# Kernel tuning notes

Measured on AMD Instinct MI355X. Metric: run time of the kernel, lower is better.

Reference implementation:

```python
import jax, jax.numpy as jnp
import numpy as np

ORDINAL = 2.0
EPS_INNER = 1e-32 * float(1.0 / ORDINAL < 1.0)  # added to inv_covar**2 (active: 0.5 < 1)
EPS_OUTER = 1e-32 * float(ORDINAL < 1.0)        # inactive for ordinal=2

def setup_inputs() -> dict:
    key = jax.random.key(0)
    k1, k2, k3, k4, k5 = jax.random.split(key, 5)
    B, I, O = 1024, 512, 512
    s = I
    inputs = jax.random.normal(k1, (B, I), dtype=jnp.float32)
    # kaiming-uniform-ish weights, small biases, centers ~ N(0, 0.1), inv_covars ~ U(1/(s+.5), 1/(s-.5))
    bound_w = float(np.sqrt(6.0 / ((1 + 5.0) * I)))
    weights = jax.random.uniform(k2, (O, I), dtype=jnp.float32, minval=-bound_w, maxval=bound_w)
    bound_b = 1.0 / float(np.sqrt(I))
    biases = jax.random.uniform(k3, (O,), dtype=jnp.float32, minval=-bound_b, maxval=bound_b)
    centers = 0.1 * jax.random.normal(k4, (O, I), dtype=jnp.float32)
    inv_covars = jax.random.uniform(k5, (O, I), dtype=jnp.float32,
                                    minval=1.0 / (s + 0.5), maxval=1.0 / (s - 0.5))
    return {"inputs": inputs, "weights": weights, "biases": biases,
            "centers": centers, "inv_covars": inv_covars}

def reference(inputs, weights, biases, centers, inv_covars):
    # linear part: [B, O]
    l = jnp.einsum('bi,oi->bo', inputs, weights) + biases
    # diag covariance Mahalanobis-like distance, general-ordinal form
    scale = jnp.power(inv_covars * inv_covars + EPS_INNER, 1.0 / ORDINAL)  # [O, I]
    # [B, O, I] broadcasted elementwise chain (memory-bound)
    d = jnp.abs(inputs[:, None, :] - centers[None, :, :]) * scale[None, :, :]
    g = jnp.sum(jnp.power(d + EPS_OUTER, ORDINAL), axis=-1)  # [B, O]
    return l * jnp.exp(-g)
```

## Files before the change

### kernel.cpp

```cpp
#include <hip/hip_runtime.h>


typedef __bf16 bf16x8 __attribute__((ext_vector_type(8)));
typedef unsigned short u16x8 __attribute__((ext_vector_type(8)));
typedef float f32x4 __attribute__((ext_vector_type(4)));

#define B_DIM 1024
#define I_DIM 512
#define O_DIM 512


__device__ __forceinline__ unsigned short f2bf(float f) {
  unsigned u = __float_as_uint(f);
  u += 0x7fffu + ((u >> 16) & 1u);
  return (unsigned short)(u >> 16);
}

__global__ __launch_bounds__(256) void prep_kernel(
    const float* __restrict__ xin, const float* __restrict__ win,
    const float* __restrict__ cin, const float* __restrict__ icin,
    unsigned short* __restrict__ xf, unsigned short* __restrict__ x2f,
    unsigned short* __restrict__ wf, unsigned short* __restrict__ scf,
    unsigned short* __restrict__ s2f) {
  int g = blockIdx.x * 256 + threadIdx.x;
  int kind, sg;
  if (g < 65536)      { kind = 0; sg = g; }
  else if (g < 98304) { kind = 1; sg = g - 65536; }
  else                { kind = 2; sg = g - 98304; }
  int rt = sg >> 10, rem = sg & 1023, ks = rem >> 6, l = rem & 63;
  int src = ((rt << 4) + (l & 15)) * I_DIM + (ks << 5) + ((l >> 4) << 3);
  int dst = sg * 8;
  if (kind == 0) {
    f32x4 a = *reinterpret_cast<const f32x4*>(xin + src);
    f32x4 b = *reinterpret_cast<const f32x4*>(xin + src + 4);
    u16x8 o1, o2;
#pragma unroll
    for (int j = 0; j < 4; j++) {
      o1[j] = f2bf(a[j]);      o1[j + 4] = f2bf(b[j]);
      o2[j] = f2bf(a[j]*a[j]); o2[j + 4] = f2bf(b[j]*b[j]);
    }
    *reinterpret_cast<u16x8*>(xf + dst)  = o1;
    *reinterpret_cast<u16x8*>(x2f + dst) = o2;
  } else if (kind == 1) {
    f32x4 a = *reinterpret_cast<const f32x4*>(win + src);
    f32x4 b = *reinterpret_cast<const f32x4*>(win + src + 4);
    u16x8 o1;
#pragma unroll
    for (int j = 0; j < 4; j++) { o1[j] = f2bf(a[j]); o1[j + 4] = f2bf(b[j]); }
    *reinterpret_cast<u16x8*>(wf + dst) = o1;
  } else {
    f32x4 c0 = *reinterpret_cast<const f32x4*>(cin + src);
    f32x4 c1 = *reinterpret_cast<const f32x4*>(cin + src + 4);
    f32x4 q0 = *reinterpret_cast<const f32x4*>(icin + src);
    f32x4 q1 = *reinterpret_cast<const f32x4*>(icin + src + 4);
    u16x8 osc, os2;
#pragma unroll
    for (int j = 0; j < 4; j++) {
      float s2a = q0[j]*q0[j] + 1e-32f;
      float s2b = q1[j]*q1[j] + 1e-32f;
      osc[j] = f2bf(s2a * c0[j]); osc[j + 4] = f2bf(s2b * c1[j]);
      os2[j] = f2bf(s2a);         os2[j + 4] = f2bf(s2b);
    }
    *reinterpret_cast<u16x8*>(scf + dst) = osc;
    *reinterpret_cast<u16x8*>(s2f + dst) = os2;
  }
}

__global__ __launch_bounds__(64) void prep_k_kernel(
    const float* __restrict__ cin, const float* __restrict__ icin,
    float* __restrict__ kvec) {
  int o = blockIdx.x, l = threadIdx.x;
  int base = o * I_DIM + l * 8;
  f32x4 c0 = *reinterpret_cast<const f32x4*>(cin + base);
  f32x4 c1 = *reinterpret_cast<const f32x4*>(cin + base + 4);
  f32x4 q0 = *reinterpret_cast<const f32x4*>(icin + base);
  f32x4 q1 = *reinterpret_cast<const f32x4*>(icin + base + 4);
  float s = 0.f;
#pragma unroll
  for (int j = 0; j < 4; j++) {
    float s2a = q0[j]*q0[j] + 1e-32f;
    float s2b = q1[j]*q1[j] + 1e-32f;
    s += s2a * c0[j] * c0[j] + s2b * c1[j] * c1[j];
  }
#pragma unroll
  for (int d = 32; d >= 1; d >>= 1) s += __shfl_xor(s, d, 64);
  if (l == 0) kvec[o] = s;
}

__global__ __launch_bounds__(64) void gemm_kernel(
    const unsigned short* __restrict__ xf, const unsigned short* __restrict__ x2f,
    const unsigned short* __restrict__ wf, const unsigned short* __restrict__ scf,
    const unsigned short* __restrict__ s2f, const float* __restrict__ kvec,
    const float* __restrict__ bias, float* __restrict__ out) {
  const int l = threadIdx.x;
  const int MT = blockIdx.x;
  const int NT = blockIdx.y;
  const int lo = l * 8;

  const unsigned short* xb[2]  = { xf  + (2*MT    ) * 8192 + lo, xf  + (2*MT + 1) * 8192 + lo };
  const unsigned short* x2b[2] = { x2f + (2*MT    ) * 8192 + lo, x2f + (2*MT + 1) * 8192 + lo };
  const unsigned short* wb[2]  = { wf  + (2*NT    ) * 8192 + lo, wf  + (2*NT + 1) * 8192 + lo };
  const unsigned short* scb[2] = { scf + (2*NT    ) * 8192 + lo, scf + (2*NT + 1) * 8192 + lo };
  const unsigned short* s2b[2] = { s2f + (2*NT    ) * 8192 + lo, s2f + (2*NT + 1) * 8192 + lo };

  f32x4 accL[2][2], accA[2][2], accB[2][2];
#pragma unroll
  for (int m = 0; m < 2; m++)
#pragma unroll
    for (int n = 0; n < 2; n++) {
      accL[m][n] = (f32x4)(0.f); accA[m][n] = (f32x4)(0.f); accB[m][n] = (f32x4)(0.f);
    }

#pragma unroll
  for (int ks = 0; ks < 16; ks++) {
    const int off = ks * 512;
    bf16x8 xa[2], x2a[2], wfr[2], scfr[2], s2fr[2];
#pragma unroll
    for (int m = 0; m < 2; m++) {
      xa[m]  = *reinterpret_cast<const bf16x8*>(xb[m]  + off);
      x2a[m] = *reinterpret_cast<const bf16x8*>(x2b[m] + off);
    }
#pragma unroll
    for (int n = 0; n < 2; n++) {
      wfr[n]  = *reinterpret_cast<const bf16x8*>(wb[n]  + off);
      scfr[n] = *reinterpret_cast<const bf16x8*>(scb[n] + off);
      s2fr[n] = *reinterpret_cast<const bf16x8*>(s2b[n] + off);
    }
#pragma unroll
    for (int m = 0; m < 2; m++)
#pragma unroll
      for (int n = 0; n < 2; n++) {
        accL[m][n] = __builtin_amdgcn_mfma_f32_16x16x32_bf16(xa[m],  wfr[n],  accL[m][n], 0, 0, 0);
        accA[m][n] = __builtin_amdgcn_mfma_f32_16x16x32_bf16(xa[m],  scfr[n], accA[m][n], 0, 0, 0);
        accB[m][n] = __builtin_amdgcn_mfma_f32_16x16x32_bf16(x2a[m], s2fr[n], accB[m][n], 0, 0, 0);
      }
  }

  const int rbase = (l >> 4) << 2;
  const int cq = l & 15;
#pragma unroll
  for (int n = 0; n < 2; n++) {
    const int ocol = NT * 32 + n * 16 + cq;
    const float bv = bias[ocol];
    const float kv = kvec[ocol];
#pragma unroll
    for (int m = 0; m < 2; m++) {
      const int orow0 = MT * 32 + m * 16 + rbase;
#pragma unroll
      for (int r = 0; r < 4; r++) {
        float g = accB[m][n][r] - 2.0f * accA[m][n][r] + kv;
        out[(orow0 + r) * O_DIM + ocol] = (accL[m][n][r] + bv) * __expf(-g);
      }
    }
  }
}

extern "C" void kernel_launch(void* const* d_in, const int* in_sizes, int n_in,
                              void* d_out, int out_size, void* d_ws, size_t ws_size,
                              hipStream_t stream) {
  const float* xin  = (const float*)d_in[0];
  const float* win  = (const float*)d_in[1];
  const float* bias = (const float*)d_in[2];
  const float* cin  = (const float*)d_in[3];
  const float* icin = (const float*)d_in[4];
  float* out = (float*)d_out;

  unsigned short* ws  = (unsigned short*)d_ws;
  unsigned short* xf  = ws;
  unsigned short* x2f = xf  + 524288;
  unsigned short* wf  = x2f + 524288;
  unsigned short* scf = wf  + 262144;
  unsigned short* s2f = scf + 262144;
  float* kvec = (float*)(s2f + 262144);

  prep_kernel<<<512, 256, 0, stream>>>(xin, win, cin, icin, xf, x2f, wf, scf, s2f);
  prep_k_kernel<<<512, 64, 0, stream>>>(cin, icin, kvec);
  gemm_kernel<<<dim3(32, 16), 64, 0, stream>>>(xf, x2f, wf, scf, s2f, kvec, bias, out);
}
```

Baseline: 76.48 us.

## Fuse kvec prep into prep kernel and halve GEMM output tile width

Computes the per-output constant kvec inside the main prep kernel using extra blocks, removing a separate kernel launch. The GEMM tile drops from 32x32 to 32x16 outputs per wave, doubling the grid to 1024 blocks for better CU occupancy. In exchange, each x/x^2 fragment is reloaded by twice as many blocks, raising global/L2 traffic per output.

```diff
diff --git a/kernel.cpp b/kernel.cpp
--- a/kernel.cpp
+++ b/kernel.cpp
@@ -21,8 +21,28 @@
     const float* __restrict__ cin, const float* __restrict__ icin,
     unsigned short* __restrict__ xf, unsigned short* __restrict__ x2f,
     unsigned short* __restrict__ wf, unsigned short* __restrict__ scf,
-    unsigned short* __restrict__ s2f) {
+    unsigned short* __restrict__ s2f, float* __restrict__ kvec) {
   int g = blockIdx.x * 256 + threadIdx.x;
+  if (g >= 131072) {
+    int o = (g - 131072) >> 6;
+    int l = g & 63;
+    int base = o * I_DIM + l * 8;
+    f32x4 c0 = *reinterpret_cast<const f32x4*>(cin + base);
+    f32x4 c1 = *reinterpret_cast<const f32x4*>(cin + base + 4);
+    f32x4 q0 = *reinterpret_cast<const f32x4*>(icin + base);
+    f32x4 q1 = *reinterpret_cast<const f32x4*>(icin + base + 4);
+    float s = 0.f;
+#pragma unroll
+    for (int j = 0; j < 4; j++) {
+      float s2a = q0[j]*q0[j] + 1e-32f;
+      float s2b = q1[j]*q1[j] + 1e-32f;
+      s += s2a * c0[j] * c0[j] + s2b * c1[j] * c1[j];
+    }
+#pragma unroll
+    for (int d = 32; d >= 1; d >>= 1) s += __shfl_xor(s, d, 64);
+    if (l == 0) kvec[o] = s;
+    return;
+  }
   int kind, sg;
   if (g < 65536)      { kind = 0; sg = g; }
   else if (g < 98304) { kind = 1; sg = g - 65536; }
@@ -66,27 +86,6 @@
   }
 }
 
-__global__ __launch_bounds__(64) void prep_k_kernel(
-    const float* __restrict__ cin, const float* __restrict__ icin,
-    float* __restrict__ kvec) {
-  int o = blockIdx.x, l = threadIdx.x;
-  int base = o * I_DIM + l * 8;
-  f32x4 c0 = *reinterpret_cast<const f32x4*>(cin + base);
-  f32x4 c1 = *reinterpret_cast<const f32x4*>(cin + base + 4);
-  f32x4 q0 = *reinterpret_cast<const f32x4*>(icin + base);
-  f32x4 q1 = *reinterpret_cast<const f32x4*>(icin + base + 4);
-  float s = 0.f;
-#pragma unroll
-  for (int j = 0; j < 4; j++) {
-    float s2a = q0[j]*q0[j] + 1e-32f;
-    float s2b = q1[j]*q1[j] + 1e-32f;
-    s += s2a * c0[j] * c0[j] + s2b * c1[j] * c1[j];
-  }
-#pragma unroll
-  for (int d = 32; d >= 1; d >>= 1) s += __shfl_xor(s, d, 64);
-  if (l == 0) kvec[o] = s;
-}
-
 __global__ __launch_bounds__(64) void gemm_kernel(
     const unsigned short* __restrict__ xf, const unsigned short* __restrict__ x2f,
     const unsigned short* __restrict__ wf, const unsigned short* __restrict__ scf,
@@ -97,60 +96,50 @@
   const int NT = blockIdx.y;
   const int lo = l * 8;
 
-  const unsigned short* xb[2]  = { xf  + (2*MT    ) * 8192 + lo, xf  + (2*MT + 1) * 8192 + lo };
-  const unsigned short* x2b[2] = { x2f + (2*MT    ) * 8192 + lo, x2f + (2*MT + 1) * 8192 + lo };
-  const unsigned short* wb[2]  = { wf  + (2*NT    ) * 8192 + lo, wf  + (2*NT + 1) * 8192 + lo };
-  const unsigned short* scb[2] = { scf + (2*NT    ) * 8192 + lo, scf + (2*NT + 1) * 8192 + lo };
-  const unsigned short* s2b[2] = { s2f + (2*NT    ) * 8192 + lo, s2f + (2*NT + 1) * 8192 + lo };
+  const unsigned short* xb0  = xf  + (2*MT    ) * 8192 + lo;
+  const unsigned short* xb1  = xf  + (2*MT + 1) * 8192 + lo;
+  const unsigned short* x2b0 = x2f + (2*MT    ) * 8192 + lo;
+  const unsigned short* x2b1 = x2f + (2*MT + 1) * 8192 + lo;
+  const unsigned short* wb   = wf  + NT * 8192 + lo;
+  const unsigned short* scb  = scf + NT * 8192 + lo;
+  const unsigned short* s2b  = s2f + NT * 8192 + lo;
 
-  f32x4 accL[2][2], accA[2][2], accB[2][2];
+  f32x4 accL[2], accA[2], accB[2];
 #pragma unroll
-  for (int m = 0; m < 2; m++)
-#pragma unroll
-    for (int n = 0; n < 2; n++) {
-      accL[m][n] = (f32x4)(0.f); accA[m][n] = (f32x4)(0.f); accB[m][n] = (f32x4)(0.f);
-    }
+  for (int m = 0; m < 2; m++) {
+    accL[m] = (f32x4)(0.f); accA[m] = (f32x4)(0.f); accB[m] = (f32x4)(0.f);
+  }
 
 #pragma unroll
   for (int ks = 0; ks < 16; ks++) {
     const int off = ks * 512;
-    bf16x8 xa[2], x2a[2], wfr[2], scfr[2], s2fr[2];
-#pragma unroll
-    for (int m = 0; m < 2; m++) {
-      xa[m]  = *reinterpret_cast<const bf16x8*>(xb[m]  + off);
-      x2a[m] = *reinterpret_cast<const bf16x8*>(x2b[m] + off);
-    }
-#pragma unroll
-    for (int n = 0; n < 2; n++) {
-      wfr[n]  = *reinterpret_cast<const bf16x8*>(wb[n]  + off);
-      scfr[n] = *reinterpret_cast<const bf16x8*>(scb[n] + off);
-      s2fr[n] = *reinterpret_cast<const bf16x8*>(s2b[n] + off);
-    }
-#pragma unroll
-    for (int m = 0; m < 2; m++)
-#pragma unroll
-      for (int n = 0; n < 2; n++) {
-        accL[m][n] = __builtin_amdgcn_mfma_f32_16x16x32_bf16(xa[m],  wfr[n],  accL[m][n], 0, 0, 0);
-        accA[m][n] = __builtin_amdgcn_mfma_f32_16x16x32_bf16(xa[m],  scfr[n], accA[m][n], 0, 0, 0);
-        accB[m][n] = __builtin_amdgcn_mfma_f32_16x16x32_bf16(x2a[m], s2fr[n], accB[m][n], 0, 0, 0);
-      }
+    bf16x8 xa0  = *reinterpret_cast<const bf16x8*>(xb0  + off);
+    bf16x8 xa1  = *reinterpret_cast<const bf16x8*>(xb1  + off);
+    bf16x8 x2a0 = *reinterpret_cast<const bf16x8*>(x2b0 + off);
+    bf16x8 x2a1 = *reinterpret_cast<const bf16x8*>(x2b1 + off);
+    bf16x8 wfr  = *reinterpret_cast<const bf16x8*>(wb   + off);
+    bf16x8 scfr = *reinterpret_cast<const bf16x8*>(scb  + off);
+    bf16x8 s2fr = *reinterpret_cast<const bf16x8*>(s2b  + off);
+    accL[0] = __builtin_amdgcn_mfma_f32_16x16x32_bf16(xa0,  wfr,  accL[0], 0, 0, 0);
+    accL[1] = __builtin_amdgcn_mfma_f32_16x16x32_bf16(xa1,  wfr,  accL[1], 0, 0, 0);
+    accA[0] = __builtin_amdgcn_mfma_f32_16x16x32_bf16(xa0,  scfr, accA[0], 0, 0, 0);
+    accA[1] = __builtin_amdgcn_mfma_f32_16x16x32_bf16(xa1,  scfr, accA[1], 0, 0, 0);
+    accB[0] = __builtin_amdgcn_mfma_f32_16x16x32_bf16(x2a0, s2fr, accB[0], 0, 0, 0);
+    accB[1] = __builtin_amdgcn_mfma_f32_16x16x32_bf16(x2a1, s2fr, accB[1], 0, 0, 0);
   }
 
   const int rbase = (l >> 4) << 2;
   const int cq = l & 15;
+  const int ocol = NT * 16 + cq;
+  const float bv = bias[ocol];
+  const float kv = kvec[ocol];
 #pragma unroll
-  for (int n = 0; n < 2; n++) {
-    const int ocol = NT * 32 + n * 16 + cq;
-    const float bv = bias[ocol];
-    const float kv = kvec[ocol];
+  for (int m = 0; m < 2; m++) {
+    const int orow0 = MT * 32 + m * 16 + rbase;
 #pragma unroll
-    for (int m = 0; m < 2; m++) {
-      const int orow0 = MT * 32 + m * 16 + rbase;
-#pragma unroll
-      for (int r = 0; r < 4; r++) {
-        float g = accB[m][n][r] - 2.0f * accA[m][n][r] + kv;
-        out[(orow0 + r) * O_DIM + ocol] = (accL[m][n][r] + bv) * __expf(-g);
-      }
+    for (int r = 0; r < 4; r++) {
+      float g = accB[m][r] - 2.0f * accA[m][r] + kv;
+      out[(orow0 + r) * O_DIM + ocol] = (accL[m][r] + bv) * __expf(-g);
     }
   }
 }
@@ -173,7 +162,6 @@
   unsigned short* s2f = scf + 262144;
   float* kvec = (float*)(s2f + 262144);
 
-  prep_kernel<<<512, 256, 0, stream>>>(xin, win, cin, icin, xf, x2f, wf, scf, s2f);
-  prep_k_kernel<<<512, 64, 0, stream>>>(cin, icin, kvec);
-  gemm_kernel<<<dim3(32, 16), 64, 0, stream>>>(xf, x2f, wf, scf, s2f, kvec, bias, out);
+  prep_kernel<<<640, 256, 0, stream>>>(xin, win, cin, icin, xf, x2f, wf, scf, s2f, kvec);
+  gemm_kernel<<<dim3(32, 32), 64, 0, stream>>>(xf, x2f, wf, scf, s2f, kvec, bias, out);
 }
```

New measurement: 70.79 us. -7.4%, faster.

## Fuse bf16 conversion and center-norm reduction into the MFMA GEMM kernel

Applied to the files above, without the earlier changes.

Removes the two prep kernels and the workspace round-trip. The GEMM kernel now loads fp32 inputs, weights, centers and inverse covariances directly, converts them to bf16 in registers, and computes the per-output constant term with a wave shuffle reduction. This saves two launches and the bf16 intermediate writes and reads. In exchange every tile redundantly converts its operands and reads twice as many bytes (fp32) from L2/HBM per MFMA, and the loop unroll drops from full to 2.

```diff
diff --git a/kernel.cpp b/kernel.cpp
--- a/kernel.cpp
+++ b/kernel.cpp
@@ -2,130 +2,84 @@
 
 
 typedef __bf16 bf16x8 __attribute__((ext_vector_type(8)));
-typedef unsigned short u16x8 __attribute__((ext_vector_type(8)));
 typedef float f32x4 __attribute__((ext_vector_type(4)));
 
-#define B_DIM 1024
 #define I_DIM 512
 #define O_DIM 512
 
-
-__device__ __forceinline__ unsigned short f2bf(float f) {
-  unsigned u = __float_as_uint(f);
-  u += 0x7fffu + ((u >> 16) & 1u);
-  return (unsigned short)(u >> 16);
-}
-
-__global__ __launch_bounds__(256) void prep_kernel(
+__global__ __launch_bounds__(64) void fgn_fused_kernel(
     const float* __restrict__ xin, const float* __restrict__ win,
-    const float* __restrict__ cin, const float* __restrict__ icin,
-    unsigned short* __restrict__ xf, unsigned short* __restrict__ x2f,
-    unsigned short* __restrict__ wf, unsigned short* __restrict__ scf,
-    unsigned short* __restrict__ s2f) {
-  int g = blockIdx.x * 256 + threadIdx.x;
-  int kind, sg;
-  if (g < 65536)      { kind = 0; sg = g; }
-  else if (g < 98304) { kind = 1; sg = g - 65536; }
-  else                { kind = 2; sg = g - 98304; }
-  int rt = sg >> 10, rem = sg & 1023, ks = rem >> 6, l = rem & 63;
-  int src = ((rt << 4) + (l & 15)) * I_DIM + (ks << 5) + ((l >> 4) << 3);
-  int dst = sg * 8;
-  if (kind == 0) {
-    f32x4 a = *reinterpret_cast<const f32x4*>(xin + src);
-    f32x4 b = *reinterpret_cast<const f32x4*>(xin + src + 4);
-    u16x8 o1, o2;
-#pragma unroll
-    for (int j = 0; j < 4; j++) {
-      o1[j] = f2bf(a[j]);      o1[j + 4] = f2bf(b[j]);
-      o2[j] = f2bf(a[j]*a[j]); o2[j + 4] = f2bf(b[j]*b[j]);
-    }
-    *reinterpret_cast<u16x8*>(xf + dst)  = o1;
-    *reinterpret_cast<u16x8*>(x2f + dst) = o2;
-  } else if (kind == 1) {
-    f32x4 a = *reinterpret_cast<const f32x4*>(win + src);
-    f32x4 b = *reinterpret_cast<const f32x4*>(win + src + 4);
-    u16x8 o1;
-#pragma unroll
-    for (int j = 0; j < 4; j++) { o1[j] = f2bf(a[j]); o1[j + 4] = f2bf(b[j]); }
-    *reinterpret_cast<u16x8*>(wf + dst) = o1;
-  } else {
-    f32x4 c0 = *reinterpret_cast<const f32x4*>(cin + src);
-    f32x4 c1 = *reinterpret_cast<const f32x4*>(cin + src + 4);
-    f32x4 q0 = *reinterpret_cast<const f32x4*>(icin + src);
-    f32x4 q1 = *reinterpret_cast<const f32x4*>(icin + src + 4);
-    u16x8 osc, os2;
-#pragma unroll
-    for (int j = 0; j < 4; j++) {
-      float s2a = q0[j]*q0[j] + 1e-32f;
-      float s2b = q1[j]*q1[j] + 1e-32f;
-      osc[j] = f2bf(s2a * c0[j]); osc[j + 4] = f2bf(s2b * c1[j]);
-      os2[j] = f2bf(s2a);         os2[j + 4] = f2bf(s2b);
-    }
-    *reinterpret_cast<u16x8*>(scf + dst) = osc;
-    *reinterpret_cast<u16x8*>(s2f + dst) = os2;
-  }
-}
-
-__global__ __launch_bounds__(64) void prep_k_kernel(
-    const float* __restrict__ cin, const float* __restrict__ icin,
-    float* __restrict__ kvec) {
-  int o = blockIdx.x, l = threadIdx.x;
-  int base = o * I_DIM + l * 8;
-  f32x4 c0 = *reinterpret_cast<const f32x4*>(cin + base);
-  f32x4 c1 = *reinterpret_cast<const f32x4*>(cin + base + 4);
-  f32x4 q0 = *reinterpret_cast<const f32x4*>(icin + base);
-  f32x4 q1 = *reinterpret_cast<const f32x4*>(icin + base + 4);
-  float s = 0.f;
-#pragma unroll
-  for (int j = 0; j < 4; j++) {
-    float s2a = q0[j]*q0[j] + 1e-32f;
-    float s2b = q1[j]*q1[j] + 1e-32f;
-    s += s2a * c0[j] * c0[j] + s2b * c1[j] * c1[j];
-  }
-#pragma unroll
-  for (int d = 32; d >= 1; d >>= 1) s += __shfl_xor(s, d, 64);
-  if (l == 0) kvec[o] = s;
-}
-
-__global__ __launch_bounds__(64) void gemm_kernel(
-    const unsigned short* __restrict__ xf, const unsigned short* __restrict__ x2f,
-    const unsigned short* __restrict__ wf, const unsigned short* __restrict__ scf,
-    const unsigned short* __restrict__ s2f, const float* __restrict__ kvec,
-    const float* __restrict__ bias, float* __restrict__ out) {
-  const int l = threadIdx.x;
+    const float* __restrict__ bias, const float* __restrict__ cin,
+    const float* __restrict__ icin, float* __restrict__ out) {
+  const int l  = threadIdx.x;
+  const int li = l & 15;
+  const int lc = l >> 4;
   const int MT = blockIdx.x;
   const int NT = blockIdx.y;
-  const int lo = l * 8;
 
-  const unsigned short* xb[2]  = { xf  + (2*MT    ) * 8192 + lo, xf  + (2*MT + 1) * 8192 + lo };
-  const unsigned short* x2b[2] = { x2f + (2*MT    ) * 8192 + lo, x2f + (2*MT + 1) * 8192 + lo };
-  const unsigned short* wb[2]  = { wf  + (2*NT    ) * 8192 + lo, wf  + (2*NT + 1) * 8192 + lo };
-  const unsigned short* scb[2] = { scf + (2*NT    ) * 8192 + lo, scf + (2*NT + 1) * 8192 + lo };
-  const unsigned short* s2b[2] = { s2f + (2*NT    ) * 8192 + lo, s2f + (2*NT + 1) * 8192 + lo };
+  const int ar0 = (MT * 32 + li) * I_DIM;
+  const int ar1 = ar0 + 16 * I_DIM;
+  const int br0 = (NT * 32 + li) * I_DIM;
+  const int br1 = br0 + 16 * I_DIM;
 
   f32x4 accL[2][2], accA[2][2], accB[2][2];
 #pragma unroll
   for (int m = 0; m < 2; m++)
 #pragma unroll
     for (int n = 0; n < 2; n++) {
-      accL[m][n] = (f32x4)(0.f); accA[m][n] = (f32x4)(0.f); accB[m][n] = (f32x4)(0.f);
+      accL[m][n] = (f32x4)(0.f);
+      accA[m][n] = (f32x4)(0.f);
+      accB[m][n] = (f32x4)(0.f);
+    }
+  float kp[2] = {0.f, 0.f};
+
+#pragma unroll 2
+  for (int ks = 0; ks < 16; ks++) {
+    const int kb = ks * 32 + lc * 8;
+
+    bf16x8 xa[2], x2a[2], wfr[2], scfr[2], s2fr[2];
+
+#pragma unroll
+    for (int m = 0; m < 2; m++) {
+      const float* p = xin + (m ? ar1 : ar0) + kb;
+      f32x4 a = *reinterpret_cast<const f32x4*>(p);
+      f32x4 b = *reinterpret_cast<const f32x4*>(p + 4);
+#pragma unroll
+      for (int j = 0; j < 4; j++) {
+        xa[m][j]      = (__bf16)a[j];
+        xa[m][j + 4]  = (__bf16)b[j];
+        x2a[m][j]     = (__bf16)(a[j] * a[j]);
+        x2a[m][j + 4] = (__bf16)(b[j] * b[j]);
+      }
     }
 
 #pragma unroll
-  for (int ks = 0; ks < 16; ks++) {
-    const int off = ks * 512;
-    bf16x8 xa[2], x2a[2], wfr[2], scfr[2], s2fr[2];
+    for (int n = 0; n < 2; n++) {
+      const int rb = (n ? br1 : br0) + kb;
+      f32x4 wa = *reinterpret_cast<const f32x4*>(win + rb);
+      f32x4 wb = *reinterpret_cast<const f32x4*>(win + rb + 4);
+      f32x4 ca = *reinterpret_cast<const f32x4*>(cin + rb);
+      f32x4 cb = *reinterpret_cast<const f32x4*>(cin + rb + 4);
+      f32x4 qa = *reinterpret_cast<const f32x4*>(icin + rb);
+      f32x4 qb = *reinterpret_cast<const f32x4*>(icin + rb + 4);
+      float kacc = 0.f;
 #pragma unroll
-    for (int m = 0; m < 2; m++) {
-      xa[m]  = *reinterpret_cast<const bf16x8*>(xb[m]  + off);
-      x2a[m] = *reinterpret_cast<const bf16x8*>(x2b[m] + off);
+      for (int j = 0; j < 4; j++) {
+        wfr[n][j]     = (__bf16)wa[j];
+        wfr[n][j + 4] = (__bf16)wb[j];
+        float s2a = qa[j] * qa[j] + 1e-32f;
+        float s2b = qb[j] * qb[j] + 1e-32f;
+        float sca = s2a * ca[j];
+        float scb = s2b * cb[j];
+        scfr[n][j]     = (__bf16)sca;
+        scfr[n][j + 4] = (__bf16)scb;
+        s2fr[n][j]     = (__bf16)s2a;
+        s2fr[n][j + 4] = (__bf16)s2b;
+        kacc += sca * ca[j] + scb * cb[j];
+      }
+      kp[n] += kacc;
     }
-#pragma unroll
-    for (int n = 0; n < 2; n++) {
-      wfr[n]  = *reinterpret_cast<const bf16x8*>(wb[n]  + off);
-      scfr[n] = *reinterpret_cast<const bf16x8*>(scb[n] + off);
-      s2fr[n] = *reinterpret_cast<const bf16x8*>(s2b[n] + off);
-    }
+
 #pragma unroll
     for (int m = 0; m < 2; m++)
 #pragma unroll
@@ -136,16 +90,16 @@
       }
   }
 
-  const int rbase = (l >> 4) << 2;
-  const int cq = l & 15;
 #pragma unroll
   for (int n = 0; n < 2; n++) {
-    const int ocol = NT * 32 + n * 16 + cq;
+    float kv = kp[n];
+    kv += __shfl_xor(kv, 16, 64);
+    kv += __shfl_xor(kv, 32, 64);
+    const int ocol = NT * 32 + n * 16 + li;
     const float bv = bias[ocol];
-    const float kv = kvec[ocol];
 #pragma unroll
     for (int m = 0; m < 2; m++) {
-      const int orow0 = MT * 32 + m * 16 + rbase;
+      const int orow0 = MT * 32 + m * 16 + lc * 4;
 #pragma unroll
       for (int r = 0; r < 4; r++) {
         float g = accB[m][n][r] - 2.0f * accA[m][n][r] + kv;
@@ -164,16 +118,7 @@
   const float* cin  = (const float*)d_in[3];
   const float* icin = (const float*)d_in[4];
   float* out = (float*)d_out;
+  (void)d_ws; (void)ws_size;
 
-  unsigned short* ws  = (unsigned short*)d_ws;
-  unsigned short* xf  = ws;
-  unsigned short* x2f = xf  + 524288;
-  unsigned short* wf  = x2f + 524288;
-  unsigned short* scf = wf  + 262144;
-  unsigned short* s2f = scf + 262144;
-  float* kvec = (float*)(s2f + 262144);
-
-  prep_kernel<<<512, 256, 0, stream>>>(xin, win, cin, icin, xf, x2f, wf, scf, s2f);
-  prep_k_kernel<<<512, 64, 0, stream>>>(cin, icin, kvec);
-  gemm_kernel<<<dim3(32, 16), 64, 0, stream>>>(xf, x2f, wf, scf, s2f, kvec, bias, out);
+  fgn_fused_kernel<<<dim3(32, 16), 64, 0, stream>>>(xin, win, bias, cin, icin, out);
 }
```

Result: slower. 103.3 us (+35.0%).
